# Performance work log

Measured on AMD Instinct MI355X. Metric: run time of the kernel, lower is better.

The kernel has to match this reference:

```python
import jax, jax.numpy as jnp
import numpy as np

B, S, D = 2, 2048, 2048
H, HD = 16, 128  # n_heads, head_dim = dim // n_heads
NEG_INF = -1e9


def setup_inputs() -> dict:
    key = jax.random.key(0)
    ks = jax.random.split(key, 6)
    x = jax.random.normal(ks[0], (B, S, D), dtype=jnp.float32)
    # freqs_complex as (real, imag) pairs; unused downstream because the
    # source's apply_rotary_emb returns its input unchanged (x.type_as(x)).
    freqs_complex = jax.random.normal(ks[1], (S, HD // 2, 2), dtype=jnp.float32)
    # causal additive mask [1, 1, S, S]
    causal = jnp.tril(jnp.ones((S, S), dtype=bool))
    mask = jnp.where(causal, 0.0, NEG_INF).astype(jnp.float32)[None, None]
    wq = jax.random.normal(ks[2], (D, D), dtype=jnp.float32) * 0.02
    wk = jax.random.normal(ks[3], (D, D), dtype=jnp.float32) * 0.02
    wv = jax.random.normal(ks[4], (D, D), dtype=jnp.float32) * 0.02
    wo = jax.random.normal(ks[5], (D, D), dtype=jnp.float32) * 0.02
    return {"x": x, "freqs_complex": freqs_complex, "mask": mask,
            "wq": wq, "wk": wk, "wv": wv, "wo": wo}


def reference(x, freqs_complex, mask, wq, wk, wv, wo):
    b, s, d = x.shape
    # QKV projections (torch Linear: x @ W.T), reshape to [B, S, H, HD]
    q = (x @ wq.T).reshape(b, s, H, HD)
    k = (x @ wk.T).reshape(b, s, H, HD)
    v = (x @ wv.T).reshape(b, s, H, HD)
    # apply_rotary_emb in the source returns its input unchanged -> no-op.
    scale = 1.0 / jnp.sqrt(jnp.asarray(HD, dtype=x.dtype))
    scores = jnp.einsum('bshd,bthd->bhst', q, k) * scale + mask
    probs = jax.nn.softmax(scores.astype(jnp.float32), axis=-1).astype(q.dtype)
    out = jnp.einsum('bhst,bthd->bshd', probs, v).reshape(b, s, H * HD)
    return out @ wo.T
```

## Files before the change

### kernel.cpp

```cpp
#include <hip/hip_runtime.h>
#include <hip/hip_bf16.h>
#include <stdint.h>


namespace {

constexpr int kB = 2;
constexpr int kS = 2048;
constexpr int kD = 2048;
constexpr int kH = 16;
constexpr int kHD = 128;
constexpr int kM = kB * kS;

typedef __attribute__((ext_vector_type(8))) __bf16 bf16x8;
typedef __attribute__((ext_vector_type(4))) float f32x4;

__device__ __forceinline__ unsigned short f2bf(float x) {
  uint32_t u = __float_as_uint(x);
  u += 0x7fffu + ((u >> 16) & 1u);
  return (unsigned short)(u >> 16);
}

__device__ __forceinline__ void gld_lds16(const void* g, void* l) {
  __builtin_amdgcn_global_load_lds((__attribute__((address_space(1))) void*)g,
                                   (__attribute__((address_space(3))) void*)l,
                                   16, 0, 0);
}

__global__ void cvt_all(const float* __restrict__ x, const float* __restrict__ wq,
                        const float* __restrict__ wk, const float* __restrict__ wv,
                        const float* __restrict__ wo, unsigned short* __restrict__ xb,
                        unsigned short* __restrict__ wqkv) {
  constexpr int n4 = kD * kD / 4;
  const int i = blockIdx.x * blockDim.x + threadIdx.x;
  const int y = blockIdx.y;
  const float* src;
  unsigned short* dst;
  float s = 1.0f;
  if (y < 2) {
    src = x + (size_t)y * n4 * 4;
    dst = xb + (size_t)y * n4 * 4;
  } else {
    src = (y == 2) ? wq : (y == 3) ? wk : (y == 4) ? wv : wo;
    dst = wqkv + (size_t)(y - 2) * n4 * 4;
    if (y == 2) s = 0.08838834764831845f * 1.44269504088896340736f;
  }
  float4 v = ((const float4*)src)[i];
  ushort4 o;
  o.x = f2bf(v.x * s); o.y = f2bf(v.y * s); o.z = f2bf(v.z * s); o.w = f2bf(v.w * s);
  ((ushort4*)dst)[i] = o;
}

template <bool OUT_BF16>
__global__ __launch_bounds__(256, 2) void gemm_bt(
    const unsigned short* __restrict__ A, const unsigned short* __restrict__ W,
    void* __restrict__ C, int M, int N, int K) {
  __shared__ unsigned short Asm[128 * 64];
  __shared__ unsigned short Bsm[128 * 64];
  const int t = threadIdx.x;
  const int wave = t >> 6, lane = t & 63;
  const int ln = lane & 15, quad = lane >> 4;
  const int wr = wave >> 1, wc = wave & 1;
  const int m0 = blockIdx.y * 128, n0 = blockIdx.x * 128;

  const int srow = t >> 3;
  const int scol = ((t & 7) ^ (srow & 7)) << 3;
  const unsigned short* gA = A + (size_t)(m0 + srow) * K + scol;
  const unsigned short* gW = W + (size_t)(n0 + srow) * K + scol;
  const size_t g32 = (size_t)32 * K;
  unsigned short* lA = Asm + wave * 512;
  unsigned short* lB = Bsm + wave * 512;

  f32x4 acc[4][4] = {};

  for (int k0 = 0; k0 < K; k0 += 64) {
    __syncthreads();
#pragma unroll
    for (int i = 0; i < 4; ++i) {
      gld_lds16(gA + i * g32, lA + i * 2048);
      gld_lds16(gW + i * g32, lB + i * 2048);
    }
    gA += 64; gW += 64;
    __syncthreads();

#pragma unroll
    for (int kk = 0; kk < 2; ++kk) {
      bf16x8 af[4], bw[4];
#pragma unroll
      for (int mt = 0; mt < 4; ++mt) {
        const int row = wr * 64 + mt * 16 + ln;
        af[mt] = *(const bf16x8*)(Asm + row * 64 +
                                  (((kk * 4 + quad) ^ (row & 7)) << 3));
      }
#pragma unroll
      for (int nt = 0; nt < 4; ++nt) {
        const int row = wc * 64 + nt * 16 + ln;
        bw[nt] = *(const bf16x8*)(Bsm + row * 64 +
                                  (((kk * 4 + quad) ^ (row & 7)) << 3));
      }
#pragma unroll
      for (int mt = 0; mt < 4; ++mt)
#pragma unroll
        for (int nt = 0; nt < 4; ++nt)
          acc[mt][nt] = __builtin_amdgcn_mfma_f32_16x16x32_bf16(
              af[mt], bw[nt], acc[mt][nt], 0, 0, 0);
    }
  }

  const int cm = m0 + wr * 64 + quad * 4;
  const int cn = n0 + wc * 64 + ln;
#pragma unroll
  for (int mt = 0; mt < 4; ++mt)
#pragma unroll
    for (int r = 0; r < 4; ++r) {
      const size_t rowoff = (size_t)(cm + mt * 16 + r) * N + cn;
      if (OUT_BF16) {
        unsigned short* Cb = (unsigned short*)C;
#pragma unroll
        for (int nt = 0; nt < 4; ++nt) Cb[rowoff + nt * 16] = f2bf(acc[mt][nt][r]);
      } else {
        float* Cf = (float*)C;
#pragma unroll
        for (int nt = 0; nt < 4; ++nt) Cf[rowoff + nt * 16] = acc[mt][nt][r];
      }
    }
}

__global__ __launch_bounds__(256, 2) void gemm_qkv(
    const unsigned short* __restrict__ A, const unsigned short* __restrict__ W,
    unsigned short* __restrict__ Qb, unsigned short* __restrict__ Kb,
    unsigned short* __restrict__ Vt) {
  constexpr int K = 2048;
  __shared__ unsigned short Asm[128 * 64];
  __shared__ unsigned short Bsm[128 * 64];
  const int t = threadIdx.x;
  const int wave = t >> 6, lane = t & 63;
  const int ln = lane & 15, quad = lane >> 4;
  const int wr = wave >> 1, wc = wave & 1;
  const int m0 = blockIdx.y * 128, n0 = blockIdx.x * 128;

  const int srow = t >> 3;
  const int scol = ((t & 7) ^ (srow & 7)) << 3;
  const unsigned short* gA = A + (size_t)(m0 + srow) * K + scol;
  const unsigned short* gW = W + (size_t)(n0 + srow) * K + scol;
  const size_t g32 = (size_t)32 * K;
  unsigned short* lA = Asm + wave * 512;
  unsigned short* lB = Bsm + wave * 512;

  f32x4 acc[4][4] = {};

  for (int k0 = 0; k0 < K; k0 += 64) {
    __syncthreads();
#pragma unroll
    for (int i = 0; i < 4; ++i) {
      gld_lds16(gA + i * g32, lA + i * 2048);
      gld_lds16(gW + i * g32, lB + i * 2048);
    }
    gA += 64; gW += 64;
    __syncthreads();

#pragma unroll
    for (int kk = 0; kk < 2; ++kk) {
      bf16x8 af[4], bw[4];
#pragma unroll
      for (int mt = 0; mt < 4; ++mt) {
        const int row = wr * 64 + mt * 16 + ln;
        af[mt] = *(const bf16x8*)(Asm + row * 64 +
                                  (((kk * 4 + quad) ^ (row & 7)) << 3));
      }
#pragma unroll
      for (int nt = 0; nt < 4; ++nt) {
        const int row = wc * 64 + nt * 16 + ln;
        bw[nt] = *(const bf16x8*)(Bsm + row * 64 +
                                  (((kk * 4 + quad) ^ (row & 7)) << 3));
      }
#pragma unroll
      for (int mt = 0; mt < 4; ++mt)
#pragma unroll
        for (int nt = 0; nt < 4; ++nt)
          acc[mt][nt] = __builtin_amdgcn_mfma_f32_16x16x32_bf16(
              af[mt], bw[nt], acc[mt][nt], 0, 0, 0);
    }
  }

  const int cm = m0 + wr * 64 + quad * 4;
  const int cn = n0 + wc * 64 + ln;
  if (n0 < 4096) {
    unsigned short* dst = (n0 < 2048) ? Qb : Kb;
    const int cnl = cn & 2047;
#pragma unroll
    for (int mt = 0; mt < 4; ++mt)
#pragma unroll
      for (int r = 0; r < 4; ++r) {
        const size_t rowoff = (size_t)(cm + mt * 16 + r) * kD + cnl;
#pragma unroll
        for (int nt = 0; nt < 4; ++nt) dst[rowoff + nt * 16] = f2bf(acc[mt][nt][r]);
      }
  } else {
#pragma unroll
    for (int mt = 0; mt < 4; ++mt)
#pragma unroll
      for (int r = 0; r < 4; ++r) {
        const int m = cm + mt * 16 + r;
        const int bb = m >> 11, s = m & 2047;
#pragma unroll
        for (int nt = 0; nt < 4; ++nt) {
          const int d = cn + nt * 16 - 4096;
          Vt[((size_t)(bb * 2048 + d)) * (size_t)kS + s] = f2bf(acc[mt][nt][r]);
        }
      }
  }
}

__global__ __launch_bounds__(256, 2) void flash_attn(
    const unsigned short* __restrict__ Q, const unsigned short* __restrict__ Kb,
    const unsigned short* __restrict__ Vt, unsigned short* __restrict__ Ob) {
  __shared__ unsigned short Ksm[2][64 * 128];
  __shared__ unsigned short Vsm[2][128 * 64];
  __shared__ unsigned short Psm[4][32 * 64];
  const int t = threadIdx.x;
  const int wave = t >> 6, lane = t & 63;
  const int ln = lane & 15, quad = lane >> 4;
  const int bx = blockIdx.x;
  const int gq = bx >> 5;
  const int qt = (gq < 8) ? (15 - gq) : (gq - 8);
  const int bh = bx & 31, b = bh >> 4, h = bh & 15;
  const int q0 = qt * 128;

  bf16x8 qf[2][4];
#pragma unroll
  for (int st = 0; st < 2; ++st) {
    const size_t qoff =
        ((size_t)(b * kS + q0 + st * 64 + wave * 16 + ln)) * kD + h * kHD;
#pragma unroll
    for (int ks = 0; ks < 4; ++ks)
      qf[st][ks] = *(const bf16x8*)(Q + qoff + ks * 32 + quad * 8);
  }

  float lsum[2][4] = {};
  f32x4 oa[2][8] = {};

  const int krow = t >> 4;
  const unsigned short* gK =
      Kb + ((size_t)(b * kS) + krow) * kD + h * kHD + (((t & 15) ^ krow) << 3);
  const int vrow = t >> 3;
  const unsigned short* gV =
      Vt + ((size_t)(bh * 128 + vrow)) * kS + (((t & 7) ^ (vrow & 7)) << 3);
  unsigned short* KsmB = &Ksm[0][0];
  unsigned short* VsmB = &Vsm[0][0];

  auto stage = [&](int buf, int kv0) {
#pragma unroll
    for (int i = 0; i < 4; ++i)
      gld_lds16(gK + ((size_t)kv0 + i * 16) * kD,
                KsmB + buf * 8192 + i * 2048 + wave * 512);
#pragma unroll
    for (int i = 0; i < 4; ++i)
      gld_lds16(gV + (size_t)i * 32 * kS + kv0,
                VsmB + buf * 8192 + i * 2048 + wave * 512);
  };

  const int nIter = 2 * qt + 2;
  stage(0, 0);

  for (int it = 0; it < nIter; ++it) {
    const int kv0 = it << 6;
    const unsigned short* Ks = KsmB + (it & 1) * 8192;
    const unsigned short* Vs = VsmB + (it & 1) * 8192;
    __syncthreads();
    if (it + 1 < nIter) stage((it + 1) & 1, kv0 + 64);

    f32x4 sc[2][4] = {};
#pragma unroll
    for (int ct = 0; ct < 4; ++ct) {
      const int row = ct * 16 + ln;
#pragma unroll
      for (int ks = 0; ks < 4; ++ks) {
        bf16x8 kf =
            *(const bf16x8*)(Ks + row * 128 + (((ks * 4 + quad) ^ ln) << 3));
#pragma unroll
        for (int st = 0; st < 2; ++st)
          sc[st][ct] = __builtin_amdgcn_mfma_f32_16x16x32_bf16(
              qf[st][ks], kf, sc[st][ct], 0, 0, 0);
      }
    }

#pragma unroll
    for (int st = 0; st < 2; ++st) {
      const int q_lo = q0 + st * 64 + wave * 16;
      const bool full = (kv0 + 63 <= q_lo);
#pragma unroll
      for (int r = 0; r < 4; ++r) {
        const int qs = q_lo + quad * 4 + r;
        const int prow = st * 16 + quad * 4 + r;
        float ls = 0.0f;
#pragma unroll
        for (int ct = 0; ct < 4; ++ct) {
          float s = sc[st][ct][r];
          if (!full && (kv0 + ct * 16 + ln > qs)) s = -1e30f;
          const float p = exp2f(s);
          ls += p;
          const int slot = (ct * 2 + (ln >> 3)) ^ (prow & 7);
          Psm[wave][prow * 64 + slot * 8 + (ln & 7)] = f2bf(p);
        }
        lsum[st][r] += ls;
      }
    }

    bf16x8 pf[2][2];
#pragma unroll
    for (int st = 0; st < 2; ++st)
#pragma unroll
      for (int ks = 0; ks < 2; ++ks)
        pf[st][ks] = *(const bf16x8*)(&Psm[wave][(st * 16 + ln) * 64] +
                                      (((ks * 4 + quad) ^ (ln & 7)) << 3));
#pragma unroll
    for (int ct = 0; ct < 8; ++ct) {
      const int row = ct * 16 + ln;
#pragma unroll
      for (int ks = 0; ks < 2; ++ks) {
        bf16x8 vf =
            *(const bf16x8*)(Vs + row * 64 + (((ks * 4 + quad) ^ (ln & 7)) << 3));
#pragma unroll
        for (int st = 0; st < 2; ++st)
          oa[st][ct] = __builtin_amdgcn_mfma_f32_16x16x32_bf16(
              pf[st][ks], vf, oa[st][ct], 0, 0, 0);
      }
    }
  }

#pragma unroll
  for (int st = 0; st < 2; ++st)
#pragma unroll
    for (int r = 0; r < 4; ++r) {
      float l = lsum[st][r];
#pragma unroll
      for (int msk = 1; msk < 16; msk <<= 1) l += __shfl_xor(l, msk, 64);
      const float inv = 1.0f / l;
      const size_t orow =
          ((size_t)(b * kS + q0 + st * 64 + wave * 16 + quad * 4 + r)) * kD +
          h * kHD + ln;
#pragma unroll
      for (int ct = 0; ct < 8; ++ct) Ob[orow + ct * 16] = f2bf(oa[st][ct][r] * inv);
    }
}

}

extern "C" void kernel_launch(void* const* d_in, const int* in_sizes, int n_in,
                              void* d_out, int out_size, void* d_ws, size_t ws_size,
                              hipStream_t stream) {
  (void)in_sizes; (void)n_in; (void)out_size; (void)ws_size;
  const float* x  = (const float*)d_in[0];
  const float* wq = (const float*)d_in[3];
  const float* wk = (const float*)d_in[4];
  const float* wv = (const float*)d_in[5];
  const float* wo = (const float*)d_in[6];
  float* out = (float*)d_out;

  unsigned short* ws   = (unsigned short*)d_ws;
  unsigned short* xb   = ws;
  unsigned short* wqkv = xb + (size_t)kM * kD;
  unsigned short* wob  = wqkv + 3 * (size_t)kD * kD;
  unsigned short* Qb   = wob + (size_t)kD * kD;
  unsigned short* Kbuf = Qb  + (size_t)kM * kD;
  unsigned short* Vt   = Kbuf + (size_t)kM * kD;
  unsigned short* Ab   = Vt + (size_t)kM * kD;

  const int n4 = kD * kD / 4;
  cvt_all<<<dim3(n4 / 256, 6), 256, 0, stream>>>(x, wq, wk, wv, wo, xb, wqkv);

  gemm_qkv<<<dim3(6144 / 128, kM / 128), 256, 0, stream>>>(xb, wqkv, Qb, Kbuf, Vt);

  flash_attn<<<dim3(512), 256, 0, stream>>>(Qb, Kbuf, Vt, Ab);

  gemm_bt<false><<<dim3(kD / 128, kM / 128), 256, 0, stream>>>(Ab, wob, out, kM, kD, kD);
}
```

Measured before the change: 379.7 us.

## Double-buffer LDS tiles in projection GEMMs to overlap loads with MFMA

Both projection GEMM kernels now keep two LDS buffers for the A and W tiles. Each iteration issues the async global-to-LDS loads for the next K-tile before computing on the current one, and one barrier per iteration replaces two. The aim is to hide global memory latency behind the MFMA work. In exchange, LDS use per block doubles, which may limit occupancy. The overlap also depends on the compiler not placing a full vmcnt wait before the LDS reads.

```diff
diff --git a/kernel.cpp b/kernel.cpp
--- a/kernel.cpp
+++ b/kernel.cpp
@@ -55,8 +55,8 @@
 __global__ __launch_bounds__(256, 2) void gemm_bt(
     const unsigned short* __restrict__ A, const unsigned short* __restrict__ W,
     void* __restrict__ C, int M, int N, int K) {
-  __shared__ unsigned short Asm[128 * 64];
-  __shared__ unsigned short Bsm[128 * 64];
+  __shared__ unsigned short Asm[2][128 * 64];
+  __shared__ unsigned short Bsm[2][128 * 64];
   const int t = threadIdx.x;
   const int wave = t >> 6, lane = t & 63;
   const int ln = lane & 15, quad = lane >> 4;
@@ -68,20 +68,32 @@
   const unsigned short* gA = A + (size_t)(m0 + srow) * K + scol;
   const unsigned short* gW = W + (size_t)(n0 + srow) * K + scol;
   const size_t g32 = (size_t)32 * K;
-  unsigned short* lA = Asm + wave * 512;
-  unsigned short* lB = Bsm + wave * 512;
+  unsigned short* lA = &Asm[0][0] + wave * 512;
+  unsigned short* lB = &Bsm[0][0] + wave * 512;
 
   f32x4 acc[4][4] = {};
 
-  for (int k0 = 0; k0 < K; k0 += 64) {
+#pragma unroll
+  for (int i = 0; i < 4; ++i) {
+    gld_lds16(gA + i * g32, lA + i * 2048);
+    gld_lds16(gW + i * g32, lB + i * 2048);
+  }
+  gA += 64; gW += 64;
+
+  const int nIter = K >> 6;
+  for (int it = 0; it < nIter; ++it) {
     __syncthreads();
-#pragma unroll
-    for (int i = 0; i < 4; ++i) {
-      gld_lds16(gA + i * g32, lA + i * 2048);
-      gld_lds16(gW + i * g32, lB + i * 2048);
-    }
-    gA += 64; gW += 64;
-    __syncthreads();
+    if (it + 1 < nIter) {
+      const int nb = ((it + 1) & 1) * 8192;
+#pragma unroll
+      for (int i = 0; i < 4; ++i) {
+        gld_lds16(gA + i * g32, lA + nb + i * 2048);
+        gld_lds16(gW + i * g32, lB + nb + i * 2048);
+      }
+      gA += 64; gW += 64;
+    }
+    const unsigned short* As = &Asm[it & 1][0];
+    const unsigned short* Bs = &Bsm[it & 1][0];
 
 #pragma unroll
     for (int kk = 0; kk < 2; ++kk) {
@@ -89,13 +101,13 @@
 #pragma unroll
       for (int mt = 0; mt < 4; ++mt) {
         const int row = wr * 64 + mt * 16 + ln;
-        af[mt] = *(const bf16x8*)(Asm + row * 64 +
+        af[mt] = *(const bf16x8*)(As + row * 64 +
                                   (((kk * 4 + quad) ^ (row & 7)) << 3));
       }
 #pragma unroll
       for (int nt = 0; nt < 4; ++nt) {
         const int row = wc * 64 + nt * 16 + ln;
-        bw[nt] = *(const bf16x8*)(Bsm + row * 64 +
+        bw[nt] = *(const bf16x8*)(Bs + row * 64 +
                                   (((kk * 4 + quad) ^ (row & 7)) << 3));
       }
 #pragma unroll
@@ -131,8 +143,8 @@
     unsigned short* __restrict__ Qb, unsigned short* __restrict__ Kb,
     unsigned short* __restrict__ Vt) {
   constexpr int K = 2048;
-  __shared__ unsigned short Asm[128 * 64];
-  __shared__ unsigned short Bsm[128 * 64];
+  __shared__ unsigned short Asm[2][128 * 64];
+  __shared__ unsigned short Bsm[2][128 * 64];
   const int t = threadIdx.x;
   const int wave = t >> 6, lane = t & 63;
   const int ln = lane & 15, quad = lane >> 4;
@@ -144,20 +156,32 @@
   const unsigned short* gA = A + (size_t)(m0 + srow) * K + scol;
   const unsigned short* gW = W + (size_t)(n0 + srow) * K + scol;
   const size_t g32 = (size_t)32 * K;
-  unsigned short* lA = Asm + wave * 512;
-  unsigned short* lB = Bsm + wave * 512;
+  unsigned short* lA = &Asm[0][0] + wave * 512;
+  unsigned short* lB = &Bsm[0][0] + wave * 512;
 
   f32x4 acc[4][4] = {};
 
-  for (int k0 = 0; k0 < K; k0 += 64) {
+#pragma unroll
+  for (int i = 0; i < 4; ++i) {
+    gld_lds16(gA + i * g32, lA + i * 2048);
+    gld_lds16(gW + i * g32, lB + i * 2048);
+  }
+  gA += 64; gW += 64;
+
+  const int nIter = K >> 6;
+  for (int it = 0; it < nIter; ++it) {
     __syncthreads();
-#pragma unroll
-    for (int i = 0; i < 4; ++i) {
-      gld_lds16(gA + i * g32, lA + i * 2048);
-      gld_lds16(gW + i * g32, lB + i * 2048);
-    }
-    gA += 64; gW += 64;
-    __syncthreads();
+    if (it + 1 < nIter) {
+      const int nb = ((it + 1) & 1) * 8192;
+#pragma unroll
+      for (int i = 0; i < 4; ++i) {
+        gld_lds16(gA + i * g32, lA + nb + i * 2048);
+        gld_lds16(gW + i * g32, lB + nb + i * 2048);
+      }
+      gA += 64; gW += 64;
+    }
+    const unsigned short* As = &Asm[it & 1][0];
+    const unsigned short* Bs = &Bsm[it & 1][0];
 
 #pragma unroll
     for (int kk = 0; kk < 2; ++kk) {
@@ -165,13 +189,13 @@
 #pragma unroll
       for (int mt = 0; mt < 4; ++mt) {
         const int row = wr * 64 + mt * 16 + ln;
-        af[mt] = *(const bf16x8*)(Asm + row * 64 +
+        af[mt] = *(const bf16x8*)(As + row * 64 +
                                   (((kk * 4 + quad) ^ (row & 7)) << 3));
       }
 #pragma unroll
       for (int nt = 0; nt < 4; ++nt) {
         const int row = wc * 64 + nt * 16 + ln;
-        bw[nt] = *(const bf16x8*)(Bsm + row * 64 +
+        bw[nt] = *(const bf16x8*)(Bs + row * 64 +
                                   (((kk * 4 + quad) ^ (row & 7)) << 3));
       }
 #pragma unroll
```

New measurement: 374.0 us. Within noise of the previous version (-1.5%).

## Single-buffer attention K/V tiles and transpose score MFMA for packed P stores

Applied to the files above, without the earlier changes.

Drops the double-buffered K/V LDS staging in favour of a single buffer with load-then-sync each iteration. This cuts LDS use so three blocks per CU fit (launch bounds raised to 3), at the cost of no longer overlapping global loads with compute. The QK^T MFMA operands are swapped so each lane holds one query row and four consecutive keys. That allows packed 8-byte P stores to LDS, a per-lane row sum without the 16-lane shuffle reduction, and a rearranged swizzle.

```diff
diff --git a/kernel.cpp b/kernel.cpp
--- a/kernel.cpp
+++ b/kernel.cpp
@@ -212,12 +212,12 @@
   }
 }
 
-__global__ __launch_bounds__(256, 2) void flash_attn(
+__global__ __launch_bounds__(256, 3) void flash_attn(
     const unsigned short* __restrict__ Q, const unsigned short* __restrict__ Kb,
     const unsigned short* __restrict__ Vt, unsigned short* __restrict__ Ob) {
-  __shared__ unsigned short Ksm[2][64 * 128];
-  __shared__ unsigned short Vsm[2][128 * 64];
-  __shared__ unsigned short Psm[4][32 * 64];
+  __shared__ unsigned short Ksm[64 * 128];
+  __shared__ unsigned short Vsm[128 * 64];
+  __shared__ unsigned short Psm[4][2048];
   const int t = threadIdx.x;
   const int wave = t >> 6, lane = t & 63;
   const int ln = lane & 15, quad = lane >> 4;
@@ -237,7 +237,7 @@
       qf[st][ks] = *(const bf16x8*)(Q + qoff + ks * 32 + quad * 8);
   }
 
-  float lsum[2][4] = {};
+  float lsum[2] = {0.0f, 0.0f};
   f32x4 oa[2][8] = {};
 
   const int krow = t >> 4;
@@ -246,29 +246,19 @@
   const int vrow = t >> 3;
   const unsigned short* gV =
       Vt + ((size_t)(bh * 128 + vrow)) * kS + (((t & 7) ^ (vrow & 7)) << 3);
-  unsigned short* KsmB = &Ksm[0][0];
-  unsigned short* VsmB = &Vsm[0][0];
-
-  auto stage = [&](int buf, int kv0) {
-#pragma unroll
-    for (int i = 0; i < 4; ++i)
-      gld_lds16(gK + ((size_t)kv0 + i * 16) * kD,
-                KsmB + buf * 8192 + i * 2048 + wave * 512);
-#pragma unroll
-    for (int i = 0; i < 4; ++i)
-      gld_lds16(gV + (size_t)i * 32 * kS + kv0,
-                VsmB + buf * 8192 + i * 2048 + wave * 512);
-  };
 
   const int nIter = 2 * qt + 2;
-  stage(0, 0);
 
   for (int it = 0; it < nIter; ++it) {
     const int kv0 = it << 6;
-    const unsigned short* Ks = KsmB + (it & 1) * 8192;
-    const unsigned short* Vs = VsmB + (it & 1) * 8192;
-    __syncthreads();
-    if (it + 1 < nIter) stage((it + 1) & 1, kv0 + 64);
+    __syncthreads();
+#pragma unroll
+    for (int i = 0; i < 4; ++i)
+      gld_lds16(gK + ((size_t)kv0 + i * 16) * kD, Ksm + i * 2048 + wave * 512);
+#pragma unroll
+    for (int i = 0; i < 4; ++i)
+      gld_lds16(gV + (size_t)i * 32 * kS + kv0, Vsm + i * 2048 + wave * 512);
+    __syncthreads();
 
     f32x4 sc[2][4] = {};
 #pragma unroll
@@ -277,11 +267,11 @@
 #pragma unroll
       for (int ks = 0; ks < 4; ++ks) {
         bf16x8 kf =
-            *(const bf16x8*)(Ks + row * 128 + (((ks * 4 + quad) ^ ln) << 3));
+            *(const bf16x8*)(Ksm + row * 128 + (((ks * 4 + quad) ^ ln) << 3));
 #pragma unroll
         for (int st = 0; st < 2; ++st)
           sc[st][ct] = __builtin_amdgcn_mfma_f32_16x16x32_bf16(
-              qf[st][ks], kf, sc[st][ct], 0, 0, 0);
+              kf, qf[st][ks], sc[st][ct], 0, 0, 0);
       }
     }
 
@@ -289,22 +279,26 @@
     for (int st = 0; st < 2; ++st) {
       const int q_lo = q0 + st * 64 + wave * 16;
       const bool full = (kv0 + 63 <= q_lo);
-#pragma unroll
-      for (int r = 0; r < 4; ++r) {
-        const int qs = q_lo + quad * 4 + r;
-        const int prow = st * 16 + quad * 4 + r;
-        float ls = 0.0f;
-#pragma unroll
-        for (int ct = 0; ct < 4; ++ct) {
+      const int qs = q_lo + ln;
+      float ls = 0.0f;
+#pragma unroll
+      for (int ct = 0; ct < 4; ++ct) {
+        const int kvb = kv0 + ct * 16 + quad * 4;
+        float p[4];
+#pragma unroll
+        for (int r = 0; r < 4; ++r) {
           float s = sc[st][ct][r];
-          if (!full && (kv0 + ct * 16 + ln > qs)) s = -1e30f;
-          const float p = exp2f(s);
-          ls += p;
-          const int slot = (ct * 2 + (ln >> 3)) ^ (prow & 7);
-          Psm[wave][prow * 64 + slot * 8 + (ln & 7)] = f2bf(p);
+          if (!full && (kvb + r > qs)) s = -1e30f;
+          p[r] = exp2f(s);
+          ls += p[r];
         }
-        lsum[st][r] += ls;
-      }
+        const uint32_t u0 = (uint32_t)f2bf(p[0]) | ((uint32_t)f2bf(p[1]) << 16);
+        const uint32_t u1 = (uint32_t)f2bf(p[2]) | ((uint32_t)f2bf(p[3]) << 16);
+        const int cs = (ct * 4 + quad) ^ (ln & 14);
+        uint2 u; u.x = u0; u.y = u1;
+        *(uint2*)(&Psm[wave][(st * 16 + ln) * 64 + cs * 4]) = u;
+      }
+      lsum[st] += ls;
     }
 
     bf16x8 pf[2][2];
@@ -312,15 +306,16 @@
     for (int st = 0; st < 2; ++st)
 #pragma unroll
       for (int ks = 0; ks < 2; ++ks)
-        pf[st][ks] = *(const bf16x8*)(&Psm[wave][(st * 16 + ln) * 64] +
-                                      (((ks * 4 + quad) ^ (ln & 7)) << 3));
+        pf[st][ks] = *(const bf16x8*)(
+            &Psm[wave][(st * 16 + ln) * 64 +
+                       (((ks * 8 + quad * 2) ^ (ln & 14)) << 2)]);
 #pragma unroll
     for (int ct = 0; ct < 8; ++ct) {
       const int row = ct * 16 + ln;
 #pragma unroll
       for (int ks = 0; ks < 2; ++ks) {
         bf16x8 vf =
-            *(const bf16x8*)(Vs + row * 64 + (((ks * 4 + quad) ^ (ln & 7)) << 3));
+            *(const bf16x8*)(Vsm + row * 64 + (((ks * 4 + quad) ^ (ln & 7)) << 3));
 #pragma unroll
         for (int st = 0; st < 2; ++st)
           oa[st][ct] = __builtin_amdgcn_mfma_f32_16x16x32_bf16(
@@ -330,19 +325,23 @@
   }
 
 #pragma unroll
-  for (int st = 0; st < 2; ++st)
+  for (int st = 0; st < 2; ++st) {
+    float l = lsum[st];
+    l += __shfl_xor(l, 16, 64);
+    l += __shfl_xor(l, 32, 64);
+    float inv[4];
+#pragma unroll
+    for (int r = 0; r < 4; ++r)
+      inv[r] = 1.0f / __shfl(l, (lane & 48) | (quad * 4 + r), 64);
 #pragma unroll
     for (int r = 0; r < 4; ++r) {
-      float l = lsum[st][r];
-#pragma unroll
-      for (int msk = 1; msk < 16; msk <<= 1) l += __shfl_xor(l, msk, 64);
-      const float inv = 1.0f / l;
       const size_t orow =
           ((size_t)(b * kS + q0 + st * 64 + wave * 16 + quad * 4 + r)) * kD +
           h * kHD + ln;
 #pragma unroll
-      for (int ct = 0; ct < 8; ++ct) Ob[orow + ct * 16] = f2bf(oa[st][ct][r] * inv);
-    }
+      for (int ct = 0; ct < 8; ++ct) Ob[orow + ct * 16] = f2bf(oa[st][ct][r] * inv[r]);
+    }
+  }
 }
 
 }
```

Result: no change. 372.3 us (-2.0%).
